# Kernel tuning notes

Measured on AMD Instinct MI355X. Metric: run time of the kernel, lower is better.

Reference implementation:

```python
import jax, jax.numpy as jnp
import numpy as np

DIM = 8  # E8 lattice dimension


def _closest_Dn(x):
    """Closest point of the D_n lattice (integer vectors with even coordinate sum).
    Round every coordinate; if the sum is odd, flip the coordinate with the
    largest rounding error to its second-nearest integer. Fully vectorized
    over leading dims; last dim is the lattice dimension.
    """
    f = jnp.round(x)                     # nearest integer vector (Z^n point)
    d = x - f                            # rounding residuals in [-0.5, 0.5]
    worst = jnp.argmax(jnp.abs(d), axis=-1)            # coord with largest error
    step = jnp.where(d >= 0, 1.0, -1.0).astype(x.dtype)  # direction to 2nd-nearest int
    onehot = jax.nn.one_hot(worst, x.shape[-1], dtype=x.dtype)
    g = f + onehot * step                # f with worst coord re-rounded the other way
    odd = jnp.mod(jnp.sum(f, axis=-1), 2.0) != 0       # parity of coordinate sum
    return jnp.where(odd[..., None], g, f)


def _closest_E8(x):
    """Closest point of E8 = D8 U (D8 + 1/2): decode both cosets, keep the nearer."""
    c0 = _closest_Dn(x)                  # D8 candidate
    c1 = _closest_Dn(x - 0.5) + 0.5      # D8 + (1/2,...,1/2) candidate
    d0 = jnp.sum((x - c0) ** 2, axis=-1)
    d1 = jnp.sum((x - c1) ** 2, axis=-1)
    return jnp.where((d0 <= d1)[..., None], c0, c1)


def setup_inputs() -> dict:
    key = jax.random.key(0)
    # 4M rows of 8-dim activations; scale ~2 so points span several lattice cells
    x = jax.random.normal(key, (4000000, DIM), dtype=jnp.float32) * 2.0
    return {"x": x}


def reference(x) -> jnp.ndarray:
    # Faithful batched equivalent of the per-row closest_vector loop:
    # constrained_x[i] = E8.closest_vector(x[i]) for every row i.
    return _closest_E8(x)
```

## Files before the change

### kernel.cpp

```cpp
#include <hip/hip_runtime.h>


__global__ __launch_bounds__(256) void e8_decode_kernel(
    const float* __restrict__ x, float* __restrict__ out, int nrows) {
  #pragma clang fp contract(off)
  int stride = gridDim.x * blockDim.x;
  for (int row = blockIdx.x * blockDim.x + threadIdx.x; row < nrows; row += stride) {
    const float4* xv = reinterpret_cast<const float4*>(x) + (size_t)row * 2;
    float4 a = xv[0];
    float4 b = xv[1];
    float xr[8] = {a.x, a.y, a.z, a.w, b.x, b.y, b.z, b.w};

    float c0[8], c1[8];

    {
      float f[8], d[8];
      float sum = 0.0f;
      float best = -1.0f, dworst = 0.0f;
      int worst = 0;
      #pragma unroll
      for (int i = 0; i < 8; ++i) {
        f[i] = rintf(xr[i]);
        d[i] = xr[i] - f[i];
        float ad = fabsf(d[i]);
        if (ad > best) { best = ad; worst = i; dworst = d[i]; }
        sum += f[i];
      }
      int odd = ((int)sum) & 1;
      float step = (dworst >= 0.0f) ? 1.0f : -1.0f;
      float adj = odd ? step : 0.0f;
      #pragma unroll
      for (int i = 0; i < 8; ++i) {
        c0[i] = (i == worst) ? (f[i] + adj) : f[i];
      }
    }

    {
      float f[8], d[8];
      float sum = 0.0f;
      float best = -1.0f, dworst = 0.0f;
      int worst = 0;
      #pragma unroll
      for (int i = 0; i < 8; ++i) {
        float y = xr[i] - 0.5f;
        f[i] = rintf(y);
        d[i] = y - f[i];
        float ad = fabsf(d[i]);
        if (ad > best) { best = ad; worst = i; dworst = d[i]; }
        sum += f[i];
      }
      int odd = ((int)sum) & 1;
      float step = (dworst >= 0.0f) ? 1.0f : -1.0f;
      float adj = odd ? step : 0.0f;
      #pragma unroll
      for (int i = 0; i < 8; ++i) {
        float fi = (i == worst) ? (f[i] + adj) : f[i];
        c1[i] = fi + 0.5f;
      }
    }

    float q0[8], q1[8];
    #pragma unroll
    for (int i = 0; i < 8; ++i) {
      float r0 = xr[i] - c0[i];
      q0[i] = r0 * r0;
      float r1 = xr[i] - c1[i];
      q1[i] = r1 * r1;
    }
    float d0 = ((q0[0] + q0[1]) + (q0[2] + q0[3])) + ((q0[4] + q0[5]) + (q0[6] + q0[7]));
    float d1 = ((q1[0] + q1[1]) + (q1[2] + q1[3])) + ((q1[4] + q1[5]) + (q1[6] + q1[7]));

    bool pick0 = (d0 <= d1);
    float4 oa, ob;
    oa.x = pick0 ? c0[0] : c1[0];
    oa.y = pick0 ? c0[1] : c1[1];
    oa.z = pick0 ? c0[2] : c1[2];
    oa.w = pick0 ? c0[3] : c1[3];
    ob.x = pick0 ? c0[4] : c1[4];
    ob.y = pick0 ? c0[5] : c1[5];
    ob.z = pick0 ? c0[6] : c1[6];
    ob.w = pick0 ? c0[7] : c1[7];

    float4* ov = reinterpret_cast<float4*>(out) + (size_t)row * 2;
    ov[0] = oa;
    ov[1] = ob;
  }
}

extern "C" void kernel_launch(void* const* d_in, const int* in_sizes, int n_in,
                              void* d_out, int out_size, void* d_ws, size_t ws_size,
                              hipStream_t stream) {
  const float* x = (const float*)d_in[0];
  float* out = (float*)d_out;
  int nrows = in_sizes[0] / 8;
  int block = 256;
  int grid = (nrows + block - 1) / block;
  if (grid > 2048) grid = 2048;
  e8_decode_kernel<<<grid, block, 0, stream>>>(x, out, nrows);
}
```

Before: 223.2 us.

## Split each E8 row across lane pairs, one coset per lane, exchange via shuffles

Each thread now loads one float4 (half a row) and swaps halves with its neighbour lane, so every lane holds the full row. Even lanes decode the D8 coset and odd lanes the D8+1/2 coset. Distances and output halves are exchanged with xor shuffles, and each lane writes one float4. The grid-stride loop is replaced by one chunk per thread, which doubles thread count and makes loads fully contiguous. The cost is extra cross-lane shuffles on what is mostly a memory-bound streaming kernel.

```diff
diff --git a/kernel.cpp b/kernel.cpp
--- a/kernel.cpp
+++ b/kernel.cpp
@@ -1,89 +1,81 @@
 #include <hip/hip_runtime.h>
 
 
-__global__ __launch_bounds__(256) void e8_decode_kernel(
-    const float* __restrict__ x, float* __restrict__ out, int nrows) {
+__global__ __launch_bounds__(256) void e8_dense_kernel(
+    const float* __restrict__ x, float* __restrict__ out, int nchunks) {
   #pragma clang fp contract(off)
-  int stride = gridDim.x * blockDim.x;
-  for (int row = blockIdx.x * blockDim.x + threadIdx.x; row < nrows; row += stride) {
-    const float4* xv = reinterpret_cast<const float4*>(x) + (size_t)row * 2;
-    float4 a = xv[0];
-    float4 b = xv[1];
-    float xr[8] = {a.x, a.y, a.z, a.w, b.x, b.y, b.z, b.w};
+  int t = blockIdx.x * blockDim.x + threadIdx.x;
+  int tc = (t < nchunks) ? t : (nchunks - 1);
+  int odd_lane = t & 1;
 
-    float c0[8], c1[8];
+  const float4 mine4 = reinterpret_cast<const float4*>(x)[tc];
+  float m[4] = {mine4.x, mine4.y, mine4.z, mine4.w};
+  float th[4];
+  #pragma unroll
+  for (int k = 0; k < 4; ++k) th[k] = __shfl_xor(m[k], 1, 64);
 
-    {
-      float f[8], d[8];
-      float sum = 0.0f;
-      float best = -1.0f, dworst = 0.0f;
-      int worst = 0;
-      #pragma unroll
-      for (int i = 0; i < 8; ++i) {
-        f[i] = rintf(xr[i]);
-        d[i] = xr[i] - f[i];
-        float ad = fabsf(d[i]);
-        if (ad > best) { best = ad; worst = i; dworst = d[i]; }
-        sum += f[i];
-      }
-      int odd = ((int)sum) & 1;
-      float step = (dworst >= 0.0f) ? 1.0f : -1.0f;
-      float adj = odd ? step : 0.0f;
-      #pragma unroll
-      for (int i = 0; i < 8; ++i) {
-        c0[i] = (i == worst) ? (f[i] + adj) : f[i];
-      }
-    }
+  float xr[8];
+  #pragma unroll
+  for (int k = 0; k < 4; ++k) {
+    xr[k]     = odd_lane ? th[k] : m[k];
+    xr[k + 4] = odd_lane ? m[k]  : th[k];
+  }
 
-    {
-      float f[8], d[8];
-      float sum = 0.0f;
-      float best = -1.0f, dworst = 0.0f;
-      int worst = 0;
-      #pragma unroll
-      for (int i = 0; i < 8; ++i) {
-        float y = xr[i] - 0.5f;
-        f[i] = rintf(y);
-        d[i] = y - f[i];
-        float ad = fabsf(d[i]);
-        if (ad > best) { best = ad; worst = i; dworst = d[i]; }
-        sum += f[i];
-      }
-      int odd = ((int)sum) & 1;
-      float step = (dworst >= 0.0f) ? 1.0f : -1.0f;
-      float adj = odd ? step : 0.0f;
-      #pragma unroll
-      for (int i = 0; i < 8; ++i) {
-        float fi = (i == worst) ? (f[i] + adj) : f[i];
-        c1[i] = fi + 0.5f;
-      }
-    }
+  float h = odd_lane ? 0.5f : 0.0f;
+  float f[8];
+  float sum = 0.0f;
+  float best = -1.0f, dworst = 0.0f;
+  int worst = 0;
+  #pragma unroll
+  for (int i = 0; i < 8; ++i) {
+    float y = xr[i] - h;
+    f[i] = rintf(y);
+    float di = y - f[i];
+    float ad = fabsf(di);
+    if (ad > best) { best = ad; worst = i; dworst = di; }
+    sum += f[i];
+  }
+  int oddpar = ((int)sum) & 1;
+  float step = (dworst >= 0.0f) ? 1.0f : -1.0f;
+  float adj = oddpar ? step : 0.0f;
+  float c[8];
+  #pragma unroll
+  for (int i = 0; i < 8; ++i) {
+    float fi = (i == worst) ? (f[i] + adj) : f[i];
+    c[i] = fi + h;
+  }
 
-    float q0[8], q1[8];
-    #pragma unroll
-    for (int i = 0; i < 8; ++i) {
-      float r0 = xr[i] - c0[i];
-      q0[i] = r0 * r0;
-      float r1 = xr[i] - c1[i];
-      q1[i] = r1 * r1;
-    }
-    float d0 = ((q0[0] + q0[1]) + (q0[2] + q0[3])) + ((q0[4] + q0[5]) + (q0[6] + q0[7]));
-    float d1 = ((q1[0] + q1[1]) + (q1[2] + q1[3])) + ((q1[4] + q1[5]) + (q1[6] + q1[7]));
+  float q[8];
+  #pragma unroll
+  for (int i = 0; i < 8; ++i) {
+    float r = xr[i] - c[i];
+    q[i] = r * r;
+  }
+  float dmine = ((q[0] + q[1]) + (q[2] + q[3])) + ((q[4] + q[5]) + (q[6] + q[7]));
+  float dtheirs = __shfl_xor(dmine, 1, 64);
+  float d0 = odd_lane ? dtheirs : dmine;
+  float d1 = odd_lane ? dmine   : dtheirs;
+  bool pick0 = (d0 <= d1);
+  bool pick_own = odd_lane ? !pick0 : pick0;
 
-    bool pick0 = (d0 <= d1);
-    float4 oa, ob;
-    oa.x = pick0 ? c0[0] : c1[0];
-    oa.y = pick0 ? c0[1] : c1[1];
-    oa.z = pick0 ? c0[2] : c1[2];
-    oa.w = pick0 ? c0[3] : c1[3];
-    ob.x = pick0 ? c0[4] : c1[4];
-    ob.y = pick0 ? c0[5] : c1[5];
-    ob.z = pick0 ? c0[6] : c1[6];
-    ob.w = pick0 ? c0[7] : c1[7];
+  float send[4], recv[4];
+  #pragma unroll
+  for (int k = 0; k < 4; ++k) send[k] = odd_lane ? c[k] : c[k + 4];
+  #pragma unroll
+  for (int k = 0; k < 4; ++k) recv[k] = __shfl_xor(send[k], 1, 64);
 
-    float4* ov = reinterpret_cast<float4*>(out) + (size_t)row * 2;
-    ov[0] = oa;
-    ov[1] = ob;
+  float ownh[4];
+  #pragma unroll
+  for (int k = 0; k < 4; ++k) ownh[k] = odd_lane ? c[k + 4] : c[k];
+
+  float4 o;
+  o.x = pick_own ? ownh[0] : recv[0];
+  o.y = pick_own ? ownh[1] : recv[1];
+  o.z = pick_own ? ownh[2] : recv[2];
+  o.w = pick_own ? ownh[3] : recv[3];
+
+  if (t < nchunks) {
+    reinterpret_cast<float4*>(out)[t] = o;
   }
 }
 
@@ -92,9 +84,8 @@
                               hipStream_t stream) {
   const float* x = (const float*)d_in[0];
   float* out = (float*)d_out;
-  int nrows = in_sizes[0] / 8;
+  int nchunks = in_sizes[0] / 4;
   int block = 256;
-  int grid = (nrows + block - 1) / block;
-  if (grid > 2048) grid = 2048;
-  e8_decode_kernel<<<grid, block, 0, stream>>>(x, out, nrows);
+  int grid = (nchunks + block - 1) / block;
+  e8_dense_kernel<<<grid, block, 0, stream>>>(x, out, nchunks);
 }
```

New measurement: 226.6 us. Within noise of the previous version (+1.5%).
